# Kernel optimization log

Measured on AMD Instinct MI355X. Metric: run time of the kernel, lower is better.

Reference implementation:

```python
import jax, jax.numpy as jnp
import numpy as np

T, S, B, E, H = 1024, 1024, 4, 1024, 16
D = E // H
SCALE = D ** -0.5


def setup_inputs() -> dict:
    key = jax.random.key(0)
    ks = jax.random.split(key, 10)
    std = 0.02
    return {
        "q": jax.random.normal(ks[0], (T, B, E), jnp.float32),
        "k": jax.random.normal(ks[1], (S, B, E), jnp.float32),
        "v": jax.random.normal(ks[2], (S, B, E), jnp.float32),
        "Wq": jax.random.normal(ks[3], (E, E), jnp.float32) * std,
        "Wk": jax.random.normal(ks[4], (E, E), jnp.float32) * std,
        "Wv": jax.random.normal(ks[5], (E, E), jnp.float32) * std,
        "Wp": jax.random.normal(ks[6], (E, E), jnp.float32) * std,
        "bp": jnp.zeros((E,), jnp.float32),
        "attn_bias": jax.random.normal(ks[7], (B, H, T, S), jnp.float32) * std,
        "key_padding_mask": jax.random.bernoulli(ks[8], 0.1, (B, S)),
    }


def reference(q, k, v, Wq, Wk, Wv, Wp, bp, attn_bias, key_padding_mask):
    # projections (no bias: qkv_bias=False); torch Linear is x @ W.T
    qh = (q @ Wq.T).reshape(T, B, H, D).transpose(1, 2, 0, 3) * SCALE  # [B,H,T,D]
    kh = (k @ Wk.T).reshape(S, B, H, D).transpose(1, 2, 0, 3)          # [B,H,S,D]
    vh = (v @ Wv.T).reshape(S, B, H, D).transpose(1, 2, 0, 3)          # [B,H,S,D]

    scores = jnp.einsum("bhid,bhjd->bhij", qh, kh) + attn_bias        # [B,H,T,S]
    # detached max-subtract (as in original)
    scores = scores - jax.lax.stop_gradient(scores.max(axis=-1, keepdims=True))

    mask = key_padding_mask[:, None, None, :]                          # [B,1,1,S], True = masked
    neg = jnp.finfo(scores.dtype).min
    attn = jax.nn.softmax(jnp.where(mask, neg, scores), axis=-1)
    attn = jnp.where(mask, jnp.zeros((), scores.dtype), attn)          # XSoftmax: zero masked probs

    out = jnp.einsum("bhij,bhjd->bhid", attn, vh)                      # [B,H,T,D]
    out = out.transpose(2, 0, 1, 3).reshape(T, B, E)                   # [T,B,E]
    out = out @ Wp.T + bp                                              # output projection
    return (out, attn)
```

## Files before the change

kernel.cpp:

```cpp
#include <hip/hip_runtime.h>
#include <math.h>

constexpr int T_ = 1024, S_ = 1024, B_ = 4, E_ = 1024, H_ = 16, D_ = 64;
constexpr float SCALE_ = 0.125f;
constexpr size_t NH_ = (size_t)B_ * H_ * T_ * D_;
constexpr size_t EE_ = (size_t)E_ * E_;

typedef _Float16 h8 __attribute__((ext_vector_type(8)));
typedef _Float16 h4 __attribute__((ext_vector_type(4)));
typedef float f4 __attribute__((ext_vector_type(4)));

__device__ inline f4 mfma16(h8 a, h8 b, f4 c) {
    return __builtin_amdgcn_mfma_f32_16x16x32_f16(a, b, c, 0, 0, 0);
}

__device__ inline void gload_lds16(const void* g, void* l) {
    __builtin_amdgcn_global_load_lds(
        (const __attribute__((address_space(1))) void*)g,
        (__attribute__((address_space(3))) void*)l, 16, 0, 0);
}

__global__ __launch_bounds__(256) void cvt_all(
    const float* __restrict__ q, const float* __restrict__ k,
    const float* __restrict__ v, const float* __restrict__ wq,
    const float* __restrict__ wk, const float* __restrict__ wv,
    const float* __restrict__ wp, _Float16* __restrict__ dst)
{
    const int i8 = blockIdx.x * 256 + threadIdx.x;
    constexpr int BIG = (int)(NH_ / 8);
    constexpr int WSZ = (int)(EE_ / 8);
    const float* src;
    int loc;
    if (i8 < 3 * BIG) {
        int t = i8 / BIG; loc = i8 - t * BIG;
        src = t == 0 ? q : (t == 1 ? k : v);
    } else {
        int r = i8 - 3 * BIG;
        int t = r / WSZ; loc = r - t * WSZ;
        src = t == 0 ? wq : (t == 1 ? wk : (t == 2 ? wv : wp));
    }
    const float* p = src + (size_t)loc * 8;
    float4 a = *(const float4*)p;
    float4 b = *(const float4*)(p + 4);
    h8 o;
    o[0] = (_Float16)a.x; o[1] = (_Float16)a.y;
    o[2] = (_Float16)a.z; o[3] = (_Float16)a.w;
    o[4] = (_Float16)b.x; o[5] = (_Float16)b.y;
    o[6] = (_Float16)b.z; o[7] = (_Float16)b.w;
    *(h8*)&dst[(size_t)i8 * 8] = o;
}

template <typename EPI>
__device__ inline void gemm_core(
    const _Float16* __restrict__ A, const _Float16* __restrict__ W,
    int m0, int n0, EPI epi)
{
    __shared__ _Float16 As[64][64];
    __shared__ _Float16 Bs[128][64];

    const int tid = threadIdx.x;
    const int w = tid >> 6, l = tid & 63, lr = l & 15, lg = l >> 4;
    const int wr = w >> 2, wc = w & 3;

    const int srow = (w << 3) + (l >> 3);
    const int sg   = (l & 7) ^ (srow & 7);
    char* AsB = (char*)As;
    char* BsB = (char*)Bs;
    char* ldsA  = AsB + w * 1024;
    char* ldsB0 = BsB + w * 1024;
    char* ldsB1 = BsB + 8192 + w * 1024;

    f4 acc[2][2];
#pragma unroll
    for (int mi = 0; mi < 2; ++mi)
#pragma unroll
        for (int ni = 0; ni < 2; ++ni) acc[mi][ni] = (f4){0.f, 0.f, 0.f, 0.f};

    for (int k0 = 0; k0 < 1024; k0 += 64) {
        gload_lds16(&A[(size_t)(m0 + srow) * 1024 + k0 + sg * 8], ldsA);
        gload_lds16(&W[(size_t)(n0 + srow) * 1024 + k0 + sg * 8], ldsB0);
        gload_lds16(&W[(size_t)(n0 + 64 + srow) * 1024 + k0 + sg * 8], ldsB1);
        __syncthreads();
#pragma unroll
        for (int kk = 0; kk < 2; ++kk) {
            h8 af[2], bf[2];
#pragma unroll
            for (int mi = 0; mi < 2; ++mi) {
                int r = wr * 32 + mi * 16 + lr, kc = kk * 4 + lg;
                af[mi] = *(const h8*)(AsB + r * 128 + ((kc ^ (r & 7)) << 4));
            }
#pragma unroll
            for (int ni = 0; ni < 2; ++ni) {
                int r = wc * 32 + ni * 16 + lr, kc = kk * 4 + lg;
                bf[ni] = *(const h8*)(BsB + r * 128 + ((kc ^ (r & 7)) << 4));
            }
#pragma unroll
            for (int mi = 0; mi < 2; ++mi)
#pragma unroll
                for (int ni = 0; ni < 2; ++ni)
                    acc[mi][ni] = mfma16(af[mi], bf[ni], acc[mi][ni]);
        }
        __syncthreads();
    }

#pragma unroll
    for (int mi = 0; mi < 2; ++mi)
#pragma unroll
        for (int ni = 0; ni < 2; ++ni)
#pragma unroll
            for (int r = 0; r < 4; ++r) {
                int row = m0 + wr * 32 + mi * 16 + lg * 4 + r;
                int col = n0 + wc * 32 + ni * 16 + lr;
                epi(row, col, acc[mi][ni][r]);
            }
}

__global__ __launch_bounds__(512) void qkv_gemm(
    const _Float16* __restrict__ q16, const _Float16* __restrict__ k16,
    const _Float16* __restrict__ v16, const _Float16* __restrict__ Wq16,
    const _Float16* __restrict__ Wk16, const _Float16* __restrict__ Wv16,
    _Float16* __restrict__ qh, _Float16* __restrict__ kh,
    _Float16* __restrict__ vhT)
{
    const int z = blockIdx.z;
    const _Float16* A = z == 0 ? q16 : (z == 1 ? k16 : v16);
    const _Float16* W = z == 0 ? Wq16 : (z == 1 ? Wk16 : Wv16);
    _Float16* C = z == 0 ? qh : (z == 1 ? kh : vhT);
    const float scale = (z == 0) ? SCALE_ : 1.0f;
    const int m0 = blockIdx.x * 64, n0 = blockIdx.y * 128;

    if (z < 2) {
        gemm_core(A, W, m0, n0, [&](int row, int col, float vv) {
            int t = row >> 2, b = row & 3, h = col >> 6, d = col & 63;
            C[(((size_t)b * H_ + h) * T_ + t) * D_ + d] = (_Float16)(vv * scale);
        });
    } else {
        gemm_core(A, W, m0, n0, [&](int row, int col, float vv) {
            int s = row >> 2, b = row & 3, h = col >> 6, d = col & 63;
            C[(((size_t)b * H_ + h) * D_ + d) * S_ + s] = (_Float16)vv;
        });
    }
}

__global__ __launch_bounds__(512) void out_gemm(
    const _Float16* __restrict__ oh, const _Float16* __restrict__ Wp16,
    const float* __restrict__ bp, float* __restrict__ out)
{
    const int m0 = blockIdx.x * 64, n0 = blockIdx.y * 128;
    gemm_core(oh, Wp16, m0, n0, [&](int row, int col, float vv) {
        out[(size_t)row * E_ + col] = vv + bp[col];
    });
}

__global__ __launch_bounds__(512, 4) void fused_attn(
    const _Float16* __restrict__ qh, const _Float16* __restrict__ kh,
    const _Float16* __restrict__ vhT, const float* __restrict__ bias,
    const int* __restrict__ mask, float* __restrict__ attn,
    _Float16* __restrict__ oh)
{
    __shared__ _Float16 Pf[16 * 1024];
    __shared__ int aux_i[1024];
    __shared__ float wsum[8][16];
    char* Pb = (char*)Pf;

    const int bid = blockIdx.x;
    const int vid = (bid & 7) * 512 + (bid >> 3);
    const int bh = vid >> 6;
    const int t0 = (vid & 63) * 16;
    const int b = bh >> 4, h = bh & 15;
    const int tid = threadIdx.x;
    const int w = tid >> 6, l = tid & 63, lr = l & 15, lg = l >> 4;
    const int wbase = w * 128;

    const float* brow = bias + ((size_t)bh * T_ + t0 + lr) * S_ + wbase + lg * 4;
    f4 bv[8];
#pragma unroll
    for (int j = 0; j < 8; ++j)
        bv[j] = *(const f4*)&brow[j * 16];

    const _Float16* qbase = qh + ((size_t)bh * T_ + t0) * D_;
    h8 qf0 = *(const h8*)&qbase[(size_t)lr * D_ + lg * 8];
    h8 qf1 = *(const h8*)&qbase[(size_t)lr * D_ + 32 + lg * 8];

    for (int i = tid; i < S_; i += 512) aux_i[i] = mask[(size_t)b * S_ + i];

    asm volatile("" :: "v"(bv[0]), "v"(bv[1]), "v"(bv[2]), "v"(bv[3]),
                       "v"(bv[4]), "v"(bv[5]), "v"(bv[6]), "v"(bv[7]),
                       "v"(qf0), "v"(qf1));
    __syncthreads();

    const _Float16* kbase = kh + (size_t)bh * S_ * D_;

    f4 p[8];
    float rs = 0.f;
#pragma unroll
    for (int sub = 0; sub < 8; ++sub) {
        int s0 = wbase + sub * 16;
        h8 kf0 = *(const h8*)&kbase[(size_t)(s0 + lr) * D_ + lg * 8];
        h8 kf1 = *(const h8*)&kbase[(size_t)(s0 + lr) * D_ + 32 + lg * 8];
        f4 c = (f4){0.f, 0.f, 0.f, 0.f};
        c = mfma16(kf0, qf0, c);
        c = mfma16(kf1, qf1, c);
        int4 mv = *(const int4*)&aux_i[s0 + lg * 4];
        f4 pj;
        pj[0] = mv.x ? 0.f : __expf(c[0] + bv[sub][0]);
        pj[1] = mv.y ? 0.f : __expf(c[1] + bv[sub][1]);
        pj[2] = mv.z ? 0.f : __expf(c[2] + bv[sub][2]);
        pj[3] = mv.w ? 0.f : __expf(c[3] + bv[sub][3]);
        rs += (pj[0] + pj[1]) + (pj[2] + pj[3]);
        p[sub] = pj;
    }
    rs += __shfl_xor(rs, 16); rs += __shfl_xor(rs, 32);
    if (l < 16) wsum[w][lr] = rs;
    __syncthreads();

    float s8 = 0.f;
#pragma unroll
    for (int ww = 0; ww < 8; ++ww) s8 += wsum[ww][lr];
    const float inv = 1.0f / s8;

    float* arow = attn + ((size_t)bh * T_ + t0 + lr) * S_ + wbase + lg * 4;
#pragma unroll
    for (int sub = 0; sub < 8; ++sub) {
        f4 o = {p[sub][0] * inv, p[sub][1] * inv,
                p[sub][2] * inv, p[sub][3] * inv};
        __builtin_nontemporal_store(o, (f4*)&arow[sub * 16]);
        h4 pn;
        pn[0] = (_Float16)o[0]; pn[1] = (_Float16)o[1];
        pn[2] = (_Float16)o[2]; pn[3] = (_Float16)o[3];
        int off = (lr * 2048 + (wbase + sub * 16 + lg * 4) * 2) ^ ((lr & 7) << 4);
        *(h4*)(Pb + off) = pn;
    }
    __syncthreads();

    {
        const int sh = w & 1, dbase = (w >> 1) * 16;
        const _Float16* vbase = vhT + (size_t)bh * D_ * S_;
        f4 acc = (f4){0.f, 0.f, 0.f, 0.f};
#pragma unroll 8
        for (int kc = 0; kc < 16; ++kc) {
            int s0 = sh * 512 + kc * 32;
            int off = (lr * 2048 + (s0 + lg * 8) * 2) ^ ((lr & 7) << 4);
            h8 pf = *(const h8*)(Pb + off);
            h8 vf = *(const h8*)&vbase[(size_t)(dbase + lr) * S_ + s0 + lg * 8];
            acc = mfma16(pf, vf, acc);
        }
        float* pvred = (float*)aux_i;
        if (sh) {
#pragma unroll
            for (int r = 0; r < 4; ++r)
                pvred[(lg * 4 + r) * 64 + dbase + lr] = acc[r];
        }
        __syncthreads();
        if (!sh) {
#pragma unroll
            for (int r = 0; r < 4; ++r) {
                int t = lg * 4 + r;
                float o = acc[r] + pvred[t * 64 + dbase + lr];
                oh[((size_t)(t0 + t) * B_ + b) * E_ + h * 64 + dbase + lr] = (_Float16)o;
            }
        }
    }
}

extern "C" void kernel_launch(void* const* d_in, const int* in_sizes, int n_in,
                              void* d_out, int out_size, void* d_ws, size_t ws_size,
                              hipStream_t stream)
{
    const float* q    = (const float*)d_in[0];
    const float* k    = (const float*)d_in[1];
    const float* v    = (const float*)d_in[2];
    const float* Wq   = (const float*)d_in[3];
    const float* Wk   = (const float*)d_in[4];
    const float* Wv   = (const float*)d_in[5];
    const float* Wp   = (const float*)d_in[6];
    const float* bp   = (const float*)d_in[7];
    const float* bias = (const float*)d_in[8];
    const int*   mask = (const int*)d_in[9];

    float* out  = (float*)d_out;
    float* attn = out + (size_t)T_ * B_ * E_;

    _Float16* qh   = (_Float16*)d_ws;
    _Float16* kh   = qh + NH_;
    _Float16* vhT  = kh + NH_;
    _Float16* oh   = vhT + NH_;
    _Float16* q16  = oh + NH_;
    _Float16* k16  = q16 + NH_;
    _Float16* v16  = k16 + NH_;
    _Float16* Wq16 = v16 + NH_;
    _Float16* Wk16 = Wq16 + EE_;
    _Float16* Wv16 = Wk16 + EE_;
    _Float16* Wp16 = Wv16 + EE_;

    dim3 blk(512);

    cvt_all<<<dim3(8192), dim3(256), 0, stream>>>(q, k, v, Wq, Wk, Wv, Wp, q16);

    qkv_gemm<<<dim3(64, 8, 3), blk, 0, stream>>>(
        q16, k16, v16, Wq16, Wk16, Wv16, qh, kh, vhT);

    fused_attn<<<dim3(4096), blk, 0, stream>>>(qh, kh, vhT, bias, mask, attn, oh);

    out_gemm<<<dim3(64, 8), blk, 0, stream>>>(oh, Wp16, bp, out);
}
```

Baseline: 290.9 us.

## Fuse PV product into score loop using unnormalized probabilities per wave

Each wave now multiplies its unnormalized fp16 probabilities by V directly with 16x16x16 MFMAs inside the score loop. This removes the 32KB LDS probability buffer, one barrier and the separate PV phase. Per-wave partial outputs are reduced through LDS and divided by the row sum at the end. Bias and mask are now loaded per iteration instead of prefetched and staged in LDS, and the attn store is no longer nontemporal. Trade-offs: fp16 rounding of unnormalized exp values, more small V loads, and a larger float LDS reduction buffer.

```diff
diff --git a/kernel.cpp b/kernel.cpp
--- a/kernel.cpp
+++ b/kernel.cpp
@@ -12,6 +12,9 @@
 
 __device__ inline f4 mfma16(h8 a, h8 b, f4 c) {
     return __builtin_amdgcn_mfma_f32_16x16x32_f16(a, b, c, 0, 0, 0);
+}
+__device__ inline f4 mfma16x16(h4 a, h4 b, f4 c) {
+    return __builtin_amdgcn_mfma_f32_16x16x16f16(a, b, c, 0, 0, 0);
 }
 
 __device__ inline void gload_lds16(const void* g, void* l) {
@@ -158,10 +161,8 @@
     const int* __restrict__ mask, float* __restrict__ attn,
     _Float16* __restrict__ oh)
 {
-    __shared__ _Float16 Pf[16 * 1024];
-    __shared__ int aux_i[1024];
+    __shared__ float Ow[8][16][66];
     __shared__ float wsum[8][16];
-    char* Pb = (char*)Pf;
 
     const int bid = blockIdx.x;
     const int vid = (bid & 7) * 512 + (bid >> 3);
@@ -173,93 +174,87 @@
     const int wbase = w * 128;
 
     const float* brow = bias + ((size_t)bh * T_ + t0 + lr) * S_ + wbase + lg * 4;
-    f4 bv[8];
-#pragma unroll
-    for (int j = 0; j < 8; ++j)
-        bv[j] = *(const f4*)&brow[j * 16];
+    const int*   mrow = mask + (size_t)b * S_ + wbase + lg * 4;
+    const _Float16* kbase = kh + (size_t)bh * S_ * D_;
+    const _Float16* vbase = vhT + (size_t)bh * D_ * S_;
 
     const _Float16* qbase = qh + ((size_t)bh * T_ + t0) * D_;
     h8 qf0 = *(const h8*)&qbase[(size_t)lr * D_ + lg * 8];
     h8 qf1 = *(const h8*)&qbase[(size_t)lr * D_ + 32 + lg * 8];
 
-    for (int i = tid; i < S_; i += 512) aux_i[i] = mask[(size_t)b * S_ + i];
-
-    asm volatile("" :: "v"(bv[0]), "v"(bv[1]), "v"(bv[2]), "v"(bv[3]),
-                       "v"(bv[4]), "v"(bv[5]), "v"(bv[6]), "v"(bv[7]),
-                       "v"(qf0), "v"(qf1));
-    __syncthreads();
-
-    const _Float16* kbase = kh + (size_t)bh * S_ * D_;
-
     f4 p[8];
+    f4 opv[4];
+#pragma unroll
+    for (int db = 0; db < 4; ++db) opv[db] = (f4){0.f, 0.f, 0.f, 0.f};
     float rs = 0.f;
+
 #pragma unroll
     for (int sub = 0; sub < 8; ++sub) {
-        int s0 = wbase + sub * 16;
+        const int s0 = wbase + sub * 16;
         h8 kf0 = *(const h8*)&kbase[(size_t)(s0 + lr) * D_ + lg * 8];
         h8 kf1 = *(const h8*)&kbase[(size_t)(s0 + lr) * D_ + 32 + lg * 8];
+        f4 bv = *(const f4*)&brow[sub * 16];
+        int4 mv = *(const int4*)&mrow[sub * 16];
+
         f4 c = (f4){0.f, 0.f, 0.f, 0.f};
         c = mfma16(kf0, qf0, c);
         c = mfma16(kf1, qf1, c);
-        int4 mv = *(const int4*)&aux_i[s0 + lg * 4];
+
         f4 pj;
-        pj[0] = mv.x ? 0.f : __expf(c[0] + bv[sub][0]);
-        pj[1] = mv.y ? 0.f : __expf(c[1] + bv[sub][1]);
-        pj[2] = mv.z ? 0.f : __expf(c[2] + bv[sub][2]);
-        pj[3] = mv.w ? 0.f : __expf(c[3] + bv[sub][3]);
+        pj[0] = mv.x ? 0.f : __expf(c[0] + bv[0]);
+        pj[1] = mv.y ? 0.f : __expf(c[1] + bv[1]);
+        pj[2] = mv.z ? 0.f : __expf(c[2] + bv[2]);
+        pj[3] = mv.w ? 0.f : __expf(c[3] + bv[3]);
         rs += (pj[0] + pj[1]) + (pj[2] + pj[3]);
         p[sub] = pj;
-    }
+
+        h4 pa;
+        pa[0] = (_Float16)pj[0]; pa[1] = (_Float16)pj[1];
+        pa[2] = (_Float16)pj[2]; pa[3] = (_Float16)pj[3];
+#pragma unroll
+        for (int db = 0; db < 4; ++db) {
+            h4 vf = *(const h4*)&vbase[(size_t)(db * 16 + lr) * S_ + s0 + lg * 4];
+            opv[db] = mfma16x16(pa, vf, opv[db]);
+        }
+    }
+
     rs += __shfl_xor(rs, 16); rs += __shfl_xor(rs, 32);
     if (l < 16) wsum[w][lr] = rs;
+
+#pragma unroll
+    for (int db = 0; db < 4; ++db)
+#pragma unroll
+        for (int r = 0; r < 4; ++r)
+            Ow[w][lg * 4 + r][db * 16 + lr] = opv[db][r];
+
     __syncthreads();
 
-    float s8 = 0.f;
-#pragma unroll
-    for (int ww = 0; ww < 8; ++ww) s8 += wsum[ww][lr];
-    const float inv = 1.0f / s8;
-
-    float* arow = attn + ((size_t)bh * T_ + t0 + lr) * S_ + wbase + lg * 4;
-#pragma unroll
-    for (int sub = 0; sub < 8; ++sub) {
-        f4 o = {p[sub][0] * inv, p[sub][1] * inv,
-                p[sub][2] * inv, p[sub][3] * inv};
-        __builtin_nontemporal_store(o, (f4*)&arow[sub * 16]);
-        h4 pn;
-        pn[0] = (_Float16)o[0]; pn[1] = (_Float16)o[1];
-        pn[2] = (_Float16)o[2]; pn[3] = (_Float16)o[3];
-        int off = (lr * 2048 + (wbase + sub * 16 + lg * 4) * 2) ^ ((lr & 7) << 4);
-        *(h4*)(Pb + off) = pn;
-    }
-    __syncthreads();
-
     {
-        const int sh = w & 1, dbase = (w >> 1) * 16;
-        const _Float16* vbase = vhT + (size_t)bh * D_ * S_;
-        f4 acc = (f4){0.f, 0.f, 0.f, 0.f};
-#pragma unroll 8
-        for (int kc = 0; kc < 16; ++kc) {
-            int s0 = sh * 512 + kc * 32;
-            int off = (lr * 2048 + (s0 + lg * 8) * 2) ^ ((lr & 7) << 4);
-            h8 pf = *(const h8*)(Pb + off);
-            h8 vf = *(const h8*)&vbase[(size_t)(dbase + lr) * S_ + s0 + lg * 8];
-            acc = mfma16(pf, vf, acc);
+        float s8 = 0.f;
+#pragma unroll
+        for (int ww = 0; ww < 8; ++ww) s8 += wsum[ww][lr];
+        const float inv = 1.0f / s8;
+        float* arow = attn + ((size_t)bh * T_ + t0 + lr) * S_ + wbase + lg * 4;
+#pragma unroll
+        for (int sub = 0; sub < 8; ++sub) {
+            f4 o = {p[sub][0] * inv, p[sub][1] * inv,
+                    p[sub][2] * inv, p[sub][3] * inv};
+            *(f4*)&arow[sub * 16] = o;
         }
-        float* pvred = (float*)aux_i;
-        if (sh) {
-#pragma unroll
-            for (int r = 0; r < 4; ++r)
-                pvred[(lg * 4 + r) * 64 + dbase + lr] = acc[r];
+    }
+
+#pragma unroll
+    for (int rep = 0; rep < 2; ++rep) {
+        int idx = tid + rep * 512;
+        int t = idx >> 6, d = idx & 63;
+        float o = 0.f, s = 0.f;
+#pragma unroll
+        for (int ww = 0; ww < 8; ++ww) {
+            o += Ow[ww][t][d];
+            s += wsum[ww][t];
         }
-        __syncthreads();
-        if (!sh) {
-#pragma unroll
-            for (int r = 0; r < 4; ++r) {
-                int t = lg * 4 + r;
-                float o = acc[r] + pvred[t * 64 + dbase + lr];
-                oh[((size_t)(t0 + t) * B_ + b) * E_ + h * 64 + dbase + lr] = (_Float16)o;
-            }
-        }
+        o /= s;
+        oh[((size_t)(t0 + t) * B_ + b) * E_ + h * 64 + d] = (_Float16)o;
     }
 }
 
```

New measurement: 360.2 us. +23.8%, slower.
